# Kernel optimization log

Hardware: AMD Instinct MI355X
Metric: run time of the kernel (lower is better)

Reference implementation:

```python
import jax, jax.numpy as jnp
import numpy as np
import math

B, R, D = 2048, 512, 256
OUT = 1


def setup_inputs() -> dict:
    key = jax.random.key(0)
    k1, k2, k3, k4 = jax.random.split(key, 4)
    x = jax.random.normal(k1, (B, D), dtype=jnp.float32)
    th = jnp.zeros((R, D), dtype=jnp.float32)
    sign_param = jax.random.normal(k2, (R, D), dtype=jnp.float32) * 0.1
    mask_logit = jnp.full((R, D), -2.0, dtype=jnp.float32)
    log_kappa = jnp.asarray(math.log(6.0), dtype=jnp.float32)
    head_w = jax.random.normal(k3, (OUT, R), dtype=jnp.float32) * (1.0 / np.sqrt(R))
    head_b = jnp.zeros((OUT,), dtype=jnp.float32)
    return {"x": x, "th": th, "sign_param": sign_param,
            "mask_logit": mask_logit, "log_kappa": log_kappa,
            "head_w": head_w, "head_b": head_b}


def _corner_product_z(x, th, sign_param, mask_logit, log_kappa):
    # x: (B, D); th/sign_param/mask_logit: (R, D)
    kappa = jnp.exp(log_kappa)
    sgn = jnp.tanh(sign_param)                 # soft sign in (-1, 1), (R, D)
    # one-sided threshold predicate, broadcast to (B, R, D)
    s = jax.nn.sigmoid(kappa * sgn[None, :, :] * (x[:, None, :] - th[None, :, :]))
    m = jax.nn.sigmoid(mask_logit)             # soft feature mask, (R, D)
    gated = 1.0 - m[None, :, :] * (1.0 - s)    # masked predicate; m->0 => 1 (ignored)
    z = jnp.prod(gated, axis=-1)               # product over features -> (B, R)
    return z, s, m


def reference(x, th, sign_param, mask_logit, log_kappa, head_w, head_b):
    z, _, _ = _corner_product_z(x, th, sign_param, mask_logit, log_kappa)
    y = z @ head_w.T + head_b                  # (B, OUT)
    return y[..., 0] if OUT == 1 else y
```

## Files before the change

### kernel.cpp

```cpp
#include <hip/hip_runtime.h>
#include <math.h>

#define B_TOT 2048
#define R_TOT 512
#define D_TOT 256
#define LOG2E 1.4426950408889634f

#define D_TILE 64
#define N_TILES (D_TOT / D_TILE)
#define RULES_PER_WG 16
#define RULES_PER_WAVE 4
#define N_RG (R_TOT / RULES_PER_WG)
#define N_BG (B_TOT / 64)

__global__ __launch_bounds__(256, 4) void main_kernel(
        const float* __restrict__ x,
        const float* __restrict__ th,
        const float* __restrict__ sp,
        const float* __restrict__ ml,
        const float* __restrict__ lk,
        const float* __restrict__ head_w,
        const float* __restrict__ head_b,
        float*       __restrict__ y) {
    __shared__ float xs[D_TILE * 64];
    __shared__ float pA[RULES_PER_WG * D_TILE];
    __shared__ float pB[RULES_PER_WG * D_TILE];
    __shared__ float pM[RULES_PER_WG * D_TILE];
    __shared__ float red[256];

    const int tid  = threadIdx.x;
    const int lane = tid & 63;
    const int wave = tid >> 6;
    const int rg   = blockIdx.x;
    const int bg   = blockIdx.y;
    const int b0   = bg << 6;
    const int rbase = rg * RULES_PER_WG;

    const float kmul = -LOG2E * __builtin_amdgcn_exp2f(lk[0] * LOG2E);

    float acc[RULES_PER_WAVE];
    #pragma unroll
    for (int j = 0; j < RULES_PER_WAVE; j++) acc[j] = 1.0f;

    const float4* x4 = (const float4*)x;

    for (int dt = 0; dt < N_TILES; dt++) {
        const int dg0 = dt * D_TILE;
        if (dt) __syncthreads();

        #pragma unroll
        for (int it = 0; it < 4; it++) {
            int i  = it * 256 + tid;
            int b  = i >> 4;
            int fq = i & 15;
            float4 v = x4[(size_t)(b0 + b) * (D_TOT / 4) + dt * 16 + fq];
            int d0  = fq << 2;
            int col = b ^ (fq & 15);
            xs[(d0 + 0) * 64 + col] = v.x;
            xs[(d0 + 1) * 64 + col] = v.y;
            xs[(d0 + 2) * 64 + col] = v.z;
            xs[(d0 + 3) * 64 + col] = v.w;
        }

        #pragma unroll
        for (int it = 0; it < 4; it++) {
            int i  = it * 256 + tid;
            int rl = i >> 6;
            int dl = i & 63;
            size_t g = (size_t)(rbase + rl) * D_TOT + dg0 + dl;
            float u  = sp[g];
            float eu = __builtin_amdgcn_exp2f(2.0f * LOG2E * u);
            float t  = 1.0f - 2.0f * __builtin_amdgcn_rcpf(eu + 1.0f);
            float A  = kmul * t;
            float Bc = -A * th[g];
            float em = __builtin_amdgcn_exp2f(LOG2E * ml[g]);
            float m1 = __builtin_amdgcn_rcpf(1.0f + em);
            pA[rl * D_TILE + dl] = A;
            pB[rl * D_TILE + dl] = Bc;
            pM[rl * D_TILE + dl] = m1;
        }
        __syncthreads();

        #pragma unroll 2
        for (int dc = 0; dc < D_TILE; dc += 4) {
            int col = lane ^ ((dc >> 2) & 15);
            int xb  = dc * 64 + col;
            float xv0 = xs[xb];
            float xv1 = xs[xb + 64];
            float xv2 = xs[xb + 128];
            float xv3 = xs[xb + 192];
            #pragma unroll
            for (int j = 0; j < RULES_PER_WAVE; j++) {
                int pb = (wave * RULES_PER_WAVE + j) * D_TILE + dc;
                float4 a4 = *(const float4*)&pA[pb];
                float4 b4 = *(const float4*)&pB[pb];
                float4 m4 = *(const float4*)&pM[pb];
                float e0 = __builtin_amdgcn_exp2f(fmaf(a4.x, xv0, b4.x));
                float e1 = __builtin_amdgcn_exp2f(fmaf(a4.y, xv1, b4.y));
                float e2 = __builtin_amdgcn_exp2f(fmaf(a4.z, xv2, b4.z));
                float e3 = __builtin_amdgcn_exp2f(fmaf(a4.w, xv3, b4.w));
                float n0 = fmaf(m4.x, e0, 1.0f);
                float n1 = fmaf(m4.y, e1, 1.0f);
                float n2 = fmaf(m4.z, e2, 1.0f);
                float n3 = fmaf(m4.w, e3, 1.0f);
                float num = (n0 * n1) * (n2 * n3);
                float den = ((1.0f + e0) * (1.0f + e1)) *
                            ((1.0f + e2) * (1.0f + e3));
                acc[j] *= num * __builtin_amdgcn_rcpf(den);
            }
        }
    }

    float partial = 0.0f;
    #pragma unroll
    for (int j = 0; j < RULES_PER_WAVE; j++)
        partial = fmaf(head_w[rbase + wave * RULES_PER_WAVE + j], acc[j], partial);

    __syncthreads();
    red[tid] = partial;
    __syncthreads();
    if (wave == 0) {
        float t = red[lane] + red[64 + lane] + red[128 + lane] + red[192 + lane];
        if (rg == 0) t += head_b[0];
        atomicAdd(&y[b0 + lane], t);
    }
}

extern "C" void kernel_launch(void* const* d_in, const int* in_sizes, int n_in,
                              void* d_out, int out_size, void* d_ws, size_t ws_size,
                              hipStream_t stream) {
    const float* x  = (const float*)d_in[0];
    const float* th = (const float*)d_in[1];
    const float* sp = (const float*)d_in[2];
    const float* ml = (const float*)d_in[3];
    const float* lk = (const float*)d_in[4];
    const float* hw = (const float*)d_in[5];
    const float* hb = (const float*)d_in[6];
    float* y = (float*)d_out;

    hipMemsetAsync(y, 0, (size_t)out_size * sizeof(float), stream);
    dim3 grid(N_RG, N_BG, 1);
    main_kernel<<<grid, 256, 0, stream>>>(x, th, sp, ml, lk, hw, hb, y);
}
```

Measured before the change: 129.4 us.

## Precompute rule parameters in a prep kernel and read them wave-uniformly from global

Moves the per-(rule, feature) tanh/sigmoid parameter transform into a separate prep kernel that writes interleaved A/B/M quads to workspace. Previously every block recomputed it, 32 times per parameter across the batch groups. The main kernel now loads those parameters straight from global memory with wave-uniform float4 loads instead of staging them in LDS. It also halves rules per workgroup to 8, doubling the grid, and raises launch bounds to 8 blocks per CU. The trade-off is an extra kernel launch, workspace traffic, and reloading x tiles for twice as many workgroups.

```diff
diff --git a/kernel.cpp b/kernel.cpp
--- a/kernel.cpp
+++ b/kernel.cpp
@@ -8,46 +8,57 @@
 
 #define D_TILE 64
 #define N_TILES (D_TOT / D_TILE)
-#define RULES_PER_WG 16
-#define RULES_PER_WAVE 4
+#define RULES_PER_WG 8
+#define RULES_PER_WAVE 2
 #define N_RG (R_TOT / RULES_PER_WG)
 #define N_BG (B_TOT / 64)
 
-__global__ __launch_bounds__(256, 4) void main_kernel(
+
+__global__ void prep_kernel(const float* __restrict__ th,
+                            const float* __restrict__ sp,
+                            const float* __restrict__ ml,
+                            const float* __restrict__ lk,
+                            float* __restrict__ pp) {
+    int idx = blockIdx.x * 256 + threadIdx.x;
+    if (idx >= R_TOT * D_TOT) return;
+    float kmul = -LOG2E * __builtin_amdgcn_exp2f(lk[0] * LOG2E);
+    float u  = sp[idx];
+    float eu = __builtin_amdgcn_exp2f(2.0f * LOG2E * u);
+    float t  = 1.0f - 2.0f * __builtin_amdgcn_rcpf(eu + 1.0f);
+    float A  = kmul * t;
+    float Bc = -A * th[idx];
+    float em = __builtin_amdgcn_exp2f(LOG2E * ml[idx]);
+    float m1 = __builtin_amdgcn_rcpf(1.0f + em);
+    int r = idx >> 8, d = idx & 255;
+    int q = d >> 2, j = d & 3;
+    float* base = pp + ((size_t)r * 64 + q) * 12;
+    base[j]     = A;
+    base[4 + j] = Bc;
+    base[8 + j] = m1;
+}
+
+__global__ __launch_bounds__(256, 8) void main_kernel(
         const float* __restrict__ x,
-        const float* __restrict__ th,
-        const float* __restrict__ sp,
-        const float* __restrict__ ml,
-        const float* __restrict__ lk,
+        const float* __restrict__ pp,
         const float* __restrict__ head_w,
         const float* __restrict__ head_b,
         float*       __restrict__ y) {
     __shared__ float xs[D_TILE * 64];
-    __shared__ float pA[RULES_PER_WG * D_TILE];
-    __shared__ float pB[RULES_PER_WG * D_TILE];
-    __shared__ float pM[RULES_PER_WG * D_TILE];
     __shared__ float red[256];
 
     const int tid  = threadIdx.x;
     const int lane = tid & 63;
-    const int wave = tid >> 6;
+    const int wave = __builtin_amdgcn_readfirstlane(tid >> 6);
     const int rg   = blockIdx.x;
     const int bg   = blockIdx.y;
     const int b0   = bg << 6;
-    const int rbase = rg * RULES_PER_WG;
+    const int r0   = rg * RULES_PER_WG + wave * RULES_PER_WAVE;
 
-    const float kmul = -LOG2E * __builtin_amdgcn_exp2f(lk[0] * LOG2E);
-
-    float acc[RULES_PER_WAVE];
-    #pragma unroll
-    for (int j = 0; j < RULES_PER_WAVE; j++) acc[j] = 1.0f;
-
+    float acc0 = 1.0f, acc1 = 1.0f;
     const float4* x4 = (const float4*)x;
 
     for (int dt = 0; dt < N_TILES; dt++) {
-        const int dg0 = dt * D_TILE;
         if (dt) __syncthreads();
-
         #pragma unroll
         for (int it = 0; it < 4; it++) {
             int i  = it * 256 + tid;
@@ -55,68 +66,63 @@
             int fq = i & 15;
             float4 v = x4[(size_t)(b0 + b) * (D_TOT / 4) + dt * 16 + fq];
             int d0  = fq << 2;
-            int col = b ^ (fq & 15);
+            int col = b ^ fq;
             xs[(d0 + 0) * 64 + col] = v.x;
             xs[(d0 + 1) * 64 + col] = v.y;
             xs[(d0 + 2) * 64 + col] = v.z;
             xs[(d0 + 3) * 64 + col] = v.w;
         }
-
-        #pragma unroll
-        for (int it = 0; it < 4; it++) {
-            int i  = it * 256 + tid;
-            int rl = i >> 6;
-            int dl = i & 63;
-            size_t g = (size_t)(rbase + rl) * D_TOT + dg0 + dl;
-            float u  = sp[g];
-            float eu = __builtin_amdgcn_exp2f(2.0f * LOG2E * u);
-            float t  = 1.0f - 2.0f * __builtin_amdgcn_rcpf(eu + 1.0f);
-            float A  = kmul * t;
-            float Bc = -A * th[g];
-            float em = __builtin_amdgcn_exp2f(LOG2E * ml[g]);
-            float m1 = __builtin_amdgcn_rcpf(1.0f + em);
-            pA[rl * D_TILE + dl] = A;
-            pB[rl * D_TILE + dl] = Bc;
-            pM[rl * D_TILE + dl] = m1;
-        }
         __syncthreads();
 
+        const float* P0 = pp + ((size_t)r0 * 64 + dt * 16) * 12;
+        const float* P1 = P0 + 64 * 12;
+
         #pragma unroll 2
-        for (int dc = 0; dc < D_TILE; dc += 4) {
-            int col = lane ^ ((dc >> 2) & 15);
-            int xb  = dc * 64 + col;
+        for (int c = 0; c < 16; c++) {
+            int col = lane ^ c;
+            int xb  = (c << 2) * 64 + col;
             float xv0 = xs[xb];
             float xv1 = xs[xb + 64];
             float xv2 = xs[xb + 128];
             float xv3 = xs[xb + 192];
-            #pragma unroll
-            for (int j = 0; j < RULES_PER_WAVE; j++) {
-                int pb = (wave * RULES_PER_WAVE + j) * D_TILE + dc;
-                float4 a4 = *(const float4*)&pA[pb];
-                float4 b4 = *(const float4*)&pB[pb];
-                float4 m4 = *(const float4*)&pM[pb];
-                float e0 = __builtin_amdgcn_exp2f(fmaf(a4.x, xv0, b4.x));
-                float e1 = __builtin_amdgcn_exp2f(fmaf(a4.y, xv1, b4.y));
-                float e2 = __builtin_amdgcn_exp2f(fmaf(a4.z, xv2, b4.z));
-                float e3 = __builtin_amdgcn_exp2f(fmaf(a4.w, xv3, b4.w));
-                float n0 = fmaf(m4.x, e0, 1.0f);
-                float n1 = fmaf(m4.y, e1, 1.0f);
-                float n2 = fmaf(m4.z, e2, 1.0f);
-                float n3 = fmaf(m4.w, e3, 1.0f);
+
+            const float4* q0 = (const float4*)(P0 + c * 12);
+            const float4* q1 = (const float4*)(P1 + c * 12);
+            float4 A0 = q0[0], Bq0 = q0[1], M0 = q0[2];
+            float4 A1 = q1[0], Bq1 = q1[1], M1 = q1[2];
+
+            {
+                float e0 = __builtin_amdgcn_exp2f(fmaf(A0.x, xv0, Bq0.x));
+                float e1 = __builtin_amdgcn_exp2f(fmaf(A0.y, xv1, Bq0.y));
+                float e2 = __builtin_amdgcn_exp2f(fmaf(A0.z, xv2, Bq0.z));
+                float e3 = __builtin_amdgcn_exp2f(fmaf(A0.w, xv3, Bq0.w));
+                float n0 = fmaf(M0.x, e0, 1.0f);
+                float n1 = fmaf(M0.y, e1, 1.0f);
+                float n2 = fmaf(M0.z, e2, 1.0f);
+                float n3 = fmaf(M0.w, e3, 1.0f);
                 float num = (n0 * n1) * (n2 * n3);
                 float den = ((1.0f + e0) * (1.0f + e1)) *
                             ((1.0f + e2) * (1.0f + e3));
-                acc[j] *= num * __builtin_amdgcn_rcpf(den);
+                acc0 *= num * __builtin_amdgcn_rcpf(den);
+            }
+            {
+                float e0 = __builtin_amdgcn_exp2f(fmaf(A1.x, xv0, Bq1.x));
+                float e1 = __builtin_amdgcn_exp2f(fmaf(A1.y, xv1, Bq1.y));
+                float e2 = __builtin_amdgcn_exp2f(fmaf(A1.z, xv2, Bq1.z));
+                float e3 = __builtin_amdgcn_exp2f(fmaf(A1.w, xv3, Bq1.w));
+                float n0 = fmaf(M1.x, e0, 1.0f);
+                float n1 = fmaf(M1.y, e1, 1.0f);
+                float n2 = fmaf(M1.z, e2, 1.0f);
+                float n3 = fmaf(M1.w, e3, 1.0f);
+                float num = (n0 * n1) * (n2 * n3);
+                float den = ((1.0f + e0) * (1.0f + e1)) *
+                            ((1.0f + e2) * (1.0f + e3));
+                acc1 *= num * __builtin_amdgcn_rcpf(den);
             }
         }
     }
 
-    float partial = 0.0f;
-    #pragma unroll
-    for (int j = 0; j < RULES_PER_WAVE; j++)
-        partial = fmaf(head_w[rbase + wave * RULES_PER_WAVE + j], acc[j], partial);
-
-    __syncthreads();
+    float partial = fmaf(head_w[r0], acc0, head_w[r0 + 1] * acc1);
     red[tid] = partial;
     __syncthreads();
     if (wave == 0) {
@@ -138,7 +144,10 @@
     const float* hb = (const float*)d_in[6];
     float* y = (float*)d_out;
 
+    float* pp = (float*)d_ws;
+
     hipMemsetAsync(y, 0, (size_t)out_size * sizeof(float), stream);
+    prep_kernel<<<(R_TOT * D_TOT + 255) / 256, 256, 0, stream>>>(th, sp, ml, lk, pp);
     dim3 grid(N_RG, N_BG, 1);
-    main_kernel<<<grid, 256, 0, stream>>>(x, th, sp, ml, lk, hw, hb, y);
+    main_kernel<<<grid, 256, 0, stream>>>(x, pp, hw, hb, y);
 }
```

Result: no change. 127.0 us (-1.8%).
